# Optimization experiments

Hardware: AMD Instinct MI355X
Metric: run time of the kernel (lower is better)

The kernel has to match this reference:

```python
import jax, jax.numpy as jnp
import numpy as np

N_HEADS = 16


def setup_inputs() -> dict:
    key = jax.random.key(0)
    k1, k2, k3, k4 = jax.random.split(key, 4)
    B, T, C = 2, 2048, 1024
    x = jax.random.normal(k1, (B, T, C), dtype=jnp.float32)
    scale = 1.0 / np.sqrt(C)
    Wq = jax.random.normal(k2, (C, C), dtype=jnp.float32) * scale
    Wk = jax.random.normal(k3, (C, C), dtype=jnp.float32) * scale
    Wv = jax.random.normal(k4, (C, C), dtype=jnp.float32) * scale
    return {"x": x, "Wq": Wq, "Wk": Wk, "Wv": Wv}


def reference(x, Wq, Wk, Wv):
    B, T, C = x.shape
    H = N_HEADS
    Dh = C // H
    # Faithful to original: direct view of (B,T,C) -> (B,H,T,Dh) (no transpose)
    q = (x @ Wq.T).reshape(B, H, T, Dh)
    k = (x @ Wk.T).reshape(B, H, T, Dh)
    v = (x @ Wv.T).reshape(B, H, T, Dh)
    scores = jnp.einsum('bhqd,bhkd->bhqk', q, k) * (1.0 / (Dh ** 0.5))
    mask = jnp.tril(jnp.ones((T, T), dtype=bool))  # causal mask
    scores = jnp.where(mask, scores, -jnp.inf)
    att = jax.nn.softmax(scores, axis=-1)
    out = jnp.einsum('bhqk,bhkd->bhqd', att, v)
    return out.reshape(B, T, C)
```

## Files before the change

kernel.cpp:

```cpp
#include <hip/hip_runtime.h>
#include <hip/hip_bf16.h>
#include <stdint.h>

#define AS1 __attribute__((address_space(1)))
#define AS3 __attribute__((address_space(3)))

typedef __bf16 bf16x8 __attribute__((ext_vector_type(8)));
typedef float  f32x4  __attribute__((ext_vector_type(4)));
typedef unsigned short ushort8v __attribute__((ext_vector_type(8)));
typedef unsigned short ushort4v __attribute__((ext_vector_type(4)));
typedef short short8v __attribute__((ext_vector_type(8)));
typedef short short4v __attribute__((ext_vector_type(4)));

__device__ __forceinline__ unsigned short f2bf(float f) {
    unsigned int u = __float_as_uint(f);
    u += 0x7fffu + ((u >> 16) & 1u);
    return (unsigned short)(u >> 16);
}
__device__ __forceinline__ unsigned int pk2bf(float a, float b) {
    __hip_bfloat162 h = __float22bfloat162_rn(make_float2(a, b));
    unsigned int u;
    __builtin_memcpy(&u, &h, 4);
    return u;
}
__device__ __forceinline__ void g2lds16(const void* gp, void* lp) {
    __builtin_amdgcn_global_load_lds((AS1 void*)gp, (AS3 void*)lp, 16, 0, 0);
}
#define E2(x) __builtin_amdgcn_exp2f(x)

__global__ __launch_bounds__(256) void cast_all(const float* __restrict__ x,
                                                const float* __restrict__ w0,
                                                const float* __restrict__ w1,
                                                const float* __restrict__ w2,
                                                unsigned short* __restrict__ xb,
                                                unsigned short* __restrict__ wc) {
    int id = blockIdx.x;
    const float* s;
    unsigned short* d;
    int base;
    if (id < 4096) { s = x; d = xb; base = id; }
    else {
        int z = (id - 4096) >> 10;
        s = (z == 0) ? w0 : (z == 1) ? w1 : w2;
        d = wc + (size_t)z * 1048576;
        base = (id - 4096) & 1023;
    }
    int i = (base * 256 + threadIdx.x) * 4;
    float4 v = *(const float4*)(s + i);
    ushort4v o = { f2bf(v.x), f2bf(v.y), f2bf(v.z), f2bf(v.w) };
    *(ushort4v*)(d + i) = o;
}

#define VMW(n) asm volatile("s_waitcnt vmcnt(" #n ")" ::: "memory")
#define NOW
#define PHCORE(STG, MFMAS, ENDW) do {                                          \
    STG;                                                                       \
    __builtin_amdgcn_s_barrier();                                              \
    asm volatile("s_waitcnt lgkmcnt(0)" ::: "memory");                         \
    __builtin_amdgcn_sched_barrier(0);                                         \
    __builtin_amdgcn_s_setprio(1);                                             \
    MFMAS;                                                                     \
    __builtin_amdgcn_s_setprio(0);                                             \
    __builtin_amdgcn_sched_barrier(0);                                         \
    ENDW;                                                                      \
    __builtin_amdgcn_s_barrier();                                              \
} while (0)

#define PHA(S, CUR, STG, ENDW) do {                                            \
    const int kx_ = ((S) * 32 + quad * 8) ^ ((cl & 7) * 8);                    \
    bf16x8 af_[4];                                                             \
    _Pragma("unroll")                                                          \
    for (int m_ = 0; m_ < 4; ++m_)                                             \
        af_[m_] = *(const bf16x8*)&SA[CUR][(rowA0 + m_ * 16) * 64 + kx_];      \
    _Pragma("unroll")                                                          \
    for (int n_ = 0; n_ < 3; ++n_)                                             \
        bqr[n_] = *(const bf16x8*)&SB[CUR][(rowB0 + n_ * 16) * 64 + kx_];      \
    PHCORE(STG,                                                                \
        _Pragma("unroll")                                                      \
        for (int m_ = 0; m_ < 4; ++m_)                                         \
            _Pragma("unroll")                                                  \
            for (int n_ = 0; n_ < 3; ++n_)                                     \
                acc[m_][n_] = __builtin_amdgcn_mfma_f32_16x16x32_bf16(         \
                    af_[m_], bqr[n_], acc[m_][n_], 0, 0, 0);                   \
        , ENDW);                                                               \
} while (0)

#define PHB(S, CUR, STG, ENDW) do {                                            \
    const int kx_ = ((S) * 32 + quad * 8) ^ ((cl & 7) * 8);                    \
    bf16x8 af_[4];                                                             \
    _Pragma("unroll")                                                          \
    for (int m_ = 0; m_ < 4; ++m_)                                             \
        af_[m_] = *(const bf16x8*)&SA[CUR][(rowA0 + 64 + m_ * 16) * 64 + kx_]; \
    PHCORE(STG,                                                                \
        _Pragma("unroll")                                                      \
        for (int m_ = 0; m_ < 4; ++m_)                                         \
            _Pragma("unroll")                                                  \
            for (int n_ = 0; n_ < 3; ++n_)                                     \
                acc[4 + m_][n_] = __builtin_amdgcn_mfma_f32_16x16x32_bf16(     \
                    af_[m_], bqr[n_], acc[4 + m_][n_], 0, 0, 0);               \
        , ENDW);                                                               \
} while (0)

__global__ __launch_bounds__(512, 2) void gemm_qkv(const unsigned short* __restrict__ X,
                                                   const unsigned short* __restrict__ W,
                                                   unsigned short* __restrict__ QKV) {
    const int K = 1024;
    const int b = blockIdx.x;
    const int xcd = b & 7;
    const int j = b >> 3;
    const int m0 = (xcd * 2 + (j >> 4)) * 256;
    const int n0 = (j & 15) * 192;

    const float qs0 = 0.18033688011112042f;

    __shared__ unsigned short SA[2][16384];
    __shared__ unsigned short SB[2][12288];

    const int t = threadIdx.x;
    const int w = t >> 6;
    const int l = t & 63;
    const int cl = l & 15;
    const int quad = l >> 4;
    const int rowA0 = (w >> 2) * 128 + cl;
    const int rowB0 = (w & 3) * 48 + cl;

    const int srow8 = t >> 3;
    const int klog = (((t & 7) ^ ((t >> 3) & 7)) * 8);
    const unsigned short* Abase = X + (size_t)(m0 + srow8) * K + klog;
    const unsigned short* Bbase = W + (size_t)(n0 + srow8) * K + klog;
    unsigned short* const sa0 = &SA[0][w * 512];
    unsigned short* const sa1 = &SA[1][w * 512];
    unsigned short* const sb0 = &SB[0][w * 512];
    unsigned short* const sb1 = &SB[1][w * 512];

    f32x4 acc[8][3] = {};
    bf16x8 bqr[3];

#define STGA(nb, q, k0) g2lds16(Abase + (size_t)(q) * 65536 + (k0), ((nb) ? sa1 : sa0) + (q) * 4096)
#define STGB(nb, q, k0) g2lds16(Bbase + (size_t)(q) * 65536 + (k0), ((nb) ? sb1 : sb0) + (q) * 4096)

    STGB(0, 0, 0); STGB(0, 1, 0); STGB(0, 2, 0);
    STGA(0, 0, 0); STGA(0, 2, 0); STGA(0, 1, 0); STGA(0, 3, 0);
    VMW(2);
    __builtin_amdgcn_s_barrier();

    for (int tt = 0; tt < 15; ++tt) {
        const int cur = tt & 1, nxt = cur ^ 1;
        const int k1 = (tt + 1) * 64;
        PHA(0, cur, { STGB(nxt, 0, k1); STGB(nxt, 1, k1); }, VMW(2));
        PHB(0, cur, { STGB(nxt, 2, k1); STGA(nxt, 0, k1); }, NOW);
        PHA(1, cur, { STGA(nxt, 2, k1); STGA(nxt, 1, k1); }, NOW);
        PHB(1, cur, { STGA(nxt, 3, k1); },                   VMW(2));
    }
    PHA(0, 1, {}, VMW(0));
    PHB(0, 1, {}, NOW);
    PHA(1, 1, {}, NOW);
    PHB(1, 1, {}, NOW);

#undef STGA
#undef STGB

    #pragma unroll
    for (int mf = 0; mf < 8; ++mf) {
        #pragma unroll
        for (int rr = 0; rr < 4; ++rr) {
            size_t row = (size_t)(m0 + (w >> 2) * 128 + mf * 16 + quad * 4 + rr);
            #pragma unroll
            for (int nf = 0; nf < 3; ++nf) {
                const int nbase = n0 + (w & 3) * 48 + nf * 16;
                const int z = nbase >> 10;
                const float qs = (z == 0) ? qs0 : 1.0f;
                unsigned short* Cz = QKV + (size_t)z * 4194304;
                Cz[row * 1024 + ((nbase & 1023) + cl)] = f2bf(acc[mf][nf][rr] * qs);
            }
        }
    }
}

__global__ __launch_bounds__(256) void vtrans(const unsigned short* __restrict__ Vn,
                                              unsigned short* __restrict__ V3) {
    const int bh = blockIdx.y;
    const int T0 = blockIdx.x * 128;
    __shared__ unsigned short L[128 * 72];
    const int t = threadIdx.x;

    const unsigned short* src = Vn + (size_t)bh * 131072 + (size_t)T0 * 64;
    #pragma unroll
    for (int p = 0; p < 4; ++p) {
        int r = p * 32 + (t >> 3), c = (t & 7) * 8;
        *(ushort8v*)(L + r * 72 + c) = *(const ushort8v*)(src + (size_t)r * 64 + c);
    }
    __syncthreads();
    unsigned short* dst = V3 + (size_t)bh * 131072 + (size_t)(T0 >> 4) * 1024;
    #pragma unroll
    for (int p = 0; p < 2; ++p) {
        int item = p * 256 + t;
        int kb = item >> 6, cl = (item >> 2) & 15, qk = item & 3;
        ushort8v a, b;
        #pragma unroll
        for (int u = 0; u < 8; ++u) {
            int dt = u >> 2, j = u & 3;
            a[u] = L[(kb * 16 + qk * 4 + j) * 72 + dt * 16 + cl];
            b[u] = L[(kb * 16 + qk * 4 + j) * 72 + (dt + 2) * 16 + cl];
        }
        unsigned short* dp = dst + kb * 1024 + cl * 64 + qk * 16;
        *(ushort8v*)(dp) = a;
        *(ushort8v*)(dp + 8) = b;
    }
}

__global__ __launch_bounds__(256, 4) void attn(const unsigned short* __restrict__ QK,
                                               const unsigned short* __restrict__ V3,
                                               float* __restrict__ Out) {
    const int id = blockIdx.x;
    const int g = id & 255;
    const int s4 = id >> 8;
    const int bh = g & 31;
    const int pp = g >> 5;
    const int bb = (s4 == 0) ? (31 - pp)
                 : (s4 == 1) ? pp
                 : (s4 == 2) ? (23 - pp)
                             : (8 + pp);
    const int t = threadIdx.x;
    const int w = t >> 6;
    const int l = t & 63;
    const int cl = l & 15;
    const int quad = l >> 4;
    const int c7 = cl & 7;

    const size_t bhoff = (size_t)bh * 131072;
    const unsigned short* Qb = QK + bhoff;
    const unsigned short* Kb = QK + (size_t)4194304 + bhoff;
    const unsigned short* Vb = V3 + bhoff;
    float* Ob = Out + bhoff;

    __shared__ unsigned short KVs[2][8192];

    const int g2 = t + 256;
    const int kO1 = (t >> 3) * 64 + (((t & 7) ^ ((t >> 3) & 7)) * 8);
    const int kO2 = (g2 >> 3) * 64 + (((g2 & 7) ^ ((g2 >> 3) & 7)) * 8);
    const int wg1 = t & 63;
    const int wg2 = g2 & 63;
    const int vO1 = (t >> 6) * 512 + ((wg1 ^ ((wg1 >> 3) & 7)) * 8);
    const int vO2 = (g2 >> 6) * 512 + ((wg2 ^ ((wg2 >> 3) & 7)) * 8);
    const int lB1 = w * 512;
    const int lB2 = 2048 + w * 512;

    const int oK0 = cl * 64 + (((quad)     ^ c7) * 8);
    const int oK1 = cl * 64 + (((quad + 4) ^ c7) * 8);
    const int oV0 = cl * 64 + (((quad * 2)     ^ c7) * 8);
    const int oV1 = cl * 64 + (((quad * 2 + 1) ^ c7) * 8);

    const int mrel = w * 16 + cl;
    const int nch = bb + 1;
    const int m0w = bb * 64 + w * 16;

    bf16x8 qf0, qf1;
    {
        const unsigned short* qa = Qb + (size_t)(m0w + cl) * 64 + quad * 8;
        qf0 = *(const bf16x8*)(qa);
        qf1 = *(const bf16x8*)(qa + 32);
    }

    f32x4 o[4] = {};
    float lps = 0.f;

    {
        unsigned short* s = &KVs[0][0];
        g2lds16(Kb + kO1, s + lB1);
        g2lds16(Kb + kO2, s + lB2);
        g2lds16(Vb + vO1, s + 4096 + lB1);
        g2lds16(Vb + vO2, s + 4096 + lB2);
    }

    for (int c = 0; c < nch; ++c) {
        __syncthreads();
        if (c + 1 < nch) {
            unsigned short* s = &KVs[(c + 1) & 1][0];
            const size_t off = (size_t)(c + 1) * 4096;
            g2lds16(Kb + off + kO1, s + lB1);
            g2lds16(Kb + off + kO2, s + lB2);
            g2lds16(Vb + off + vO1, s + 4096 + lB1);
            g2lds16(Vb + off + vO2, s + 4096 + lB2);
        }
        const unsigned short* Kl = &KVs[c & 1][0];
        const unsigned short* Vl = Kl + 4096;
        const bool masked = (c == bb);

        bf16x8 kf0[4], kf1[4];
        #pragma unroll
        for (int kt = 0; kt < 4; ++kt) {
            kf0[kt] = *(const bf16x8*)(Kl + kt * 1024 + oK0);
            kf1[kt] = *(const bf16x8*)(Kl + kt * 1024 + oK1);
        }
        f32x4 st[4] = {};
        __builtin_amdgcn_s_setprio(1);
        #pragma unroll
        for (int kt = 0; kt < 4; ++kt) {
            st[kt] = __builtin_amdgcn_mfma_f32_16x16x32_bf16(kf0[kt], qf0, st[kt], 0, 0, 0);
            st[kt] = __builtin_amdgcn_mfma_f32_16x16x32_bf16(kf1[kt], qf1, st[kt], 0, 0, 0);
        }
        __builtin_amdgcn_s_setprio(0);

        short4v pb[4];
        #pragma unroll
        for (int kt = 0; kt < 4; ++kt) {
            float p0, p1, p2, p3;
            if (masked) {
                const int lk = kt * 16 + quad * 4;
                p0 = (lk     <= mrel) ? E2(st[kt][0]) : 0.f;
                p1 = (lk + 1 <= mrel) ? E2(st[kt][1]) : 0.f;
                p2 = (lk + 2 <= mrel) ? E2(st[kt][2]) : 0.f;
                p3 = (lk + 3 <= mrel) ? E2(st[kt][3]) : 0.f;
            } else {
                p0 = E2(st[kt][0]);
                p1 = E2(st[kt][1]);
                p2 = E2(st[kt][2]);
                p3 = E2(st[kt][3]);
            }
            lps += (p0 + p1) + (p2 + p3);
            uint2 u = { pk2bf(p0, p1), pk2bf(p2, p3) };
            short4v pv;
            __builtin_memcpy(&pv, &u, 8);
            pb[kt] = pv;
        }

        __builtin_amdgcn_s_setprio(1);
        #pragma unroll
        for (int kt = 0; kt < 4; ++kt) {
            short8v v0 = *(const short8v*)(Vl + kt * 1024 + oV0);
            short8v v1 = *(const short8v*)(Vl + kt * 1024 + oV1);
            short4v a0 = __builtin_shufflevector(v0, v0, 0, 1, 2, 3);
            short4v a1 = __builtin_shufflevector(v0, v0, 4, 5, 6, 7);
            short4v a2 = __builtin_shufflevector(v1, v1, 0, 1, 2, 3);
            short4v a3 = __builtin_shufflevector(v1, v1, 4, 5, 6, 7);
            o[0] = __builtin_amdgcn_mfma_f32_16x16x16bf16_1k(a0, pb[kt], o[0], 0, 0, 0);
            o[1] = __builtin_amdgcn_mfma_f32_16x16x16bf16_1k(a1, pb[kt], o[1], 0, 0, 0);
            o[2] = __builtin_amdgcn_mfma_f32_16x16x16bf16_1k(a2, pb[kt], o[2], 0, 0, 0);
            o[3] = __builtin_amdgcn_mfma_f32_16x16x16bf16_1k(a3, pb[kt], o[3], 0, 0, 0);
        }
        __builtin_amdgcn_s_setprio(0);
    }

    lps += __shfl_xor(lps, 16);
    lps += __shfl_xor(lps, 32);
    const float inv = 1.0f / lps;
    #pragma unroll
    for (int dt = 0; dt < 4; ++dt) {
        f32x4 r = o[dt];
        r[0] *= inv; r[1] *= inv; r[2] *= inv; r[3] *= inv;
        *(f32x4*)(Ob + (size_t)(m0w + cl) * 64 + dt * 16 + quad * 4) = r;
    }
}

extern "C" void kernel_launch(void* const* d_in, const int* in_sizes, int n_in,
                              void* d_out, int out_size, void* d_ws, size_t ws_size,
                              hipStream_t stream) {
    const float* x  = (const float*)d_in[0];
    const float* Wq = (const float*)d_in[1];
    const float* Wk = (const float*)d_in[2];
    const float* Wv = (const float*)d_in[3];
    float* out = (float*)d_out;

    unsigned short* xb  = (unsigned short*)d_ws;
    unsigned short* wc  = xb + (size_t)4096 * 1024;
    unsigned short* qkv = wc + (size_t)3 * 1024 * 1024;
    unsigned short* vt  = qkv + (size_t)3 * 4096 * 1024;

    hipLaunchKernelGGL(cast_all, dim3(7168), dim3(256), 0, stream, x, Wq, Wk, Wv, xb, wc);
    hipLaunchKernelGGL(gemm_qkv, dim3(256), dim3(512), 0, stream, xb, wc, qkv);
    hipLaunchKernelGGL(vtrans, dim3(16, 32), dim3(256), 0, stream, qkv + (size_t)2 * 4096 * 1024, vt);
    hipLaunchKernelGGL(attn, dim3(1024), dim3(256), 0, stream, qkv, vt, out);
}
```

Measured before the change: 138.5 us.

## Triple-buffer K/V chunks with prefetch depth two and partial vmcnt waits

Moves the attention kernel from double to triple buffering of K/V tiles in LDS. It prefetches two chunks ahead and uses partial vmcnt waits with a raw barrier instead of __syncthreads, so global-to-LDS loads have more time to land. The cost is 48KB of LDS per block and a launch bound lowered from 4 to 3 blocks per CU, which reduces occupancy.

```diff
diff --git a/kernel.cpp b/kernel.cpp
--- a/kernel.cpp
+++ b/kernel.cpp
@@ -209,7 +209,7 @@
     }
 }
 
-__global__ __launch_bounds__(256, 4) void attn(const unsigned short* __restrict__ QK,
+__global__ __launch_bounds__(256, 3) void attn(const unsigned short* __restrict__ QK,
                                                const unsigned short* __restrict__ V3,
                                                float* __restrict__ Out) {
     const int id = blockIdx.x;
@@ -234,7 +234,7 @@
     const unsigned short* Vb = V3 + bhoff;
     float* Ob = Out + bhoff;
 
-    __shared__ unsigned short KVs[2][8192];
+    __shared__ unsigned short KVs[3][8192];
 
     const int g2 = t + 256;
     const int kO1 = (t >> 3) * 64 + (((t & 7) ^ ((t >> 3) & 7)) * 8);
@@ -265,27 +265,31 @@
     f32x4 o[4] = {};
     float lps = 0.f;
 
-    {
-        unsigned short* s = &KVs[0][0];
-        g2lds16(Kb + kO1, s + lB1);
-        g2lds16(Kb + kO2, s + lB2);
-        g2lds16(Vb + vO1, s + 4096 + lB1);
-        g2lds16(Vb + vO2, s + 4096 + lB2);
-    }
-
+#define STGC(cc, buf) do {                                                     \
+    unsigned short* s_ = &KVs[buf][0];                                         \
+    const size_t off_ = (size_t)(cc) * 4096;                                   \
+    g2lds16(Kb + off_ + kO1, s_ + lB1);                                        \
+    g2lds16(Kb + off_ + kO2, s_ + lB2);                                        \
+    g2lds16(Vb + off_ + vO1, s_ + 4096 + lB1);                                 \
+    g2lds16(Vb + off_ + vO2, s_ + 4096 + lB2);                                 \
+} while (0)
+
+    STGC(0, 0);
+    if (nch > 1) STGC(1, 1);
+
+    int bc = 0;
     for (int c = 0; c < nch; ++c) {
-        __syncthreads();
-        if (c + 1 < nch) {
-            unsigned short* s = &KVs[(c + 1) & 1][0];
-            const size_t off = (size_t)(c + 1) * 4096;
-            g2lds16(Kb + off + kO1, s + lB1);
-            g2lds16(Kb + off + kO2, s + lB2);
-            g2lds16(Vb + off + vO1, s + 4096 + lB1);
-            g2lds16(Vb + off + vO2, s + 4096 + lB2);
-        }
-        const unsigned short* Kl = &KVs[c & 1][0];
+        if (c + 1 < nch) { VMW(4); } else { VMW(0); }
+        __builtin_amdgcn_s_barrier();
+        __builtin_amdgcn_sched_barrier(0);
+        if (c + 2 < nch) {
+            int bs = bc + 2 >= 3 ? bc - 1 : bc + 2;
+            STGC(c + 2, bs);
+        }
+        const unsigned short* Kl = &KVs[bc][0];
         const unsigned short* Vl = Kl + 4096;
         const bool masked = (c == bb);
+        bc = (bc == 2) ? 0 : bc + 1;
 
         bf16x8 kf0[4], kf1[4];
         #pragma unroll
@@ -341,6 +345,7 @@
         }
         __builtin_amdgcn_s_setprio(0);
     }
+#undef STGC
 
     lps += __shfl_xor(lps, 16);
     lps += __shfl_xor(lps, 32);
```

After: 139.8 us. No clear change (+1.0%).
